# Performance work log

Hardware: AMD Instinct MI355X
Metric: run time of the kernel (lower is better)

## Reference

```python
import jax, jax.numpy as jnp
import numpy as np

PACK = 8  # 32-bit words / 4-bit weights
GROUP = 128


def _unpack4(q):
    # q: [E, K//8, N] int32 packed nibbles -> [E, K, N] ints in [0, 15]
    nib = jnp.stack([(q >> (4 * j)) & 0xF for j in range(PACK)], axis=2)
    E, Kp, _, N = nib.shape
    return nib.reshape(E, Kp * PACK, N)


def _dequant(qweight, scales, g_idx):
    # GPTQ symmetric 4-bit: w = (nibble - 8) * scale[group(k), n]
    # g_idx (desc_act) maps each input row k to its quantization group,
    # equivalent math to Marlin's sorted-g_idx activation reordering.
    w = _unpack4(qweight).astype(jnp.float32) - 8.0          # [E, K, N]
    s = jnp.take_along_axis(scales, g_idx[:, :, None].astype(jnp.int32), axis=1)
    return w * s


def reference(x, router_logits, w13_qweight, w2_qweight,
              w13_scales, w2_scales, w13_g_idx, w2_g_idx, top_k):
    T = x.shape[0]
    E = w13_qweight.shape[0]
    W13 = _dequant(w13_qweight, w13_scales, w13_g_idx)   # [E, H, 2I]
    W2 = _dequant(w2_qweight, w2_scales, w2_g_idx)       # [E, I, H]
    I = W2.shape[1]

    # routing: softmax -> top-k -> renormalize
    probs = jax.nn.softmax(router_logits, axis=-1)       # [T, E]
    tw, tid = jax.lax.top_k(probs, top_k)                # [T, k]
    tw = tw / jnp.sum(tw, axis=-1, keepdims=True)
    cw = jnp.zeros((T, E), x.dtype).at[jnp.arange(T)[:, None], tid].add(tw)

    # grouped GEMM over all experts, weighted combine
    h = jnp.einsum('th,ehn->etn', x, W13)                # [E, T, 2I]
    gate, up = h[..., :I], h[..., I:]
    act = jax.nn.silu(gate) * up                         # [E, T, I]
    out_e = jnp.einsum('eti,eih->eth', act, W2)          # [E, T, H]
    return jnp.einsum('eth,te->th', out_e, cw)           # [T, H]


def setup_inputs() -> dict:
    key = jax.random.key(0)
    ks = jax.random.split(key, 8)
    T, E, H, I = 2048, 8, 1024, 4096
    x = jax.random.normal(ks[0], (T, H), dtype=jnp.float32)
    router_logits = jax.random.normal(ks[1], (T, E), dtype=jnp.float32)
    w13_qweight = jax.random.randint(ks[2], (E, H // PACK, 2 * I), 0, 2147483647, dtype=jnp.int32)
    w2_qweight = jax.random.randint(ks[3], (E, I // PACK, H), 0, 2147483647, dtype=jnp.int32)
    w13_scales = jax.random.uniform(ks[4], (E, H // GROUP, 2 * I), dtype=jnp.float32) * 0.02
    w2_scales = jax.random.uniform(ks[5], (E, I // GROUP, H), dtype=jnp.float32) * 0.02
    w13_g_idx = jax.random.randint(ks[6], (E, H), 0, H // GROUP, dtype=jnp.int32)
    w2_g_idx = jax.random.randint(ks[7], (E, I), 0, I // GROUP, dtype=jnp.int32)
    return {
        'x': x, 'router_logits': router_logits,
        'w13_qweight': w13_qweight, 'w2_qweight': w2_qweight,
        'w13_scales': w13_scales, 'w2_scales': w2_scales,
        'w13_g_idx': w13_g_idx, 'w2_g_idx': w2_g_idx,
        'top_k': 2,
    }
```

## Files before the change

### kernel.cpp

```cpp
#include <hip/hip_runtime.h>

#define T_TOK 2048
#define NEXP  8
#define H_DIM 1024
#define I_DIM 4096

#define N13  (2*I_DIM)
#define N2   (H_DIM)
#define NG13 8
#define NG2  32

#define KSPLIT2 4
#define KLEN2 (I_DIM/KSPLIT2)
#define BK   64

#define MAXT1 24
#define MAXT2 40

typedef __bf16 bf16x8 __attribute__((ext_vector_type(8)));
typedef float  f32x4  __attribute__((ext_vector_type(4)));

#define GLD_LDS(g, l) \
  __builtin_amdgcn_global_load_lds((const __attribute__((address_space(1))) void*)(g), \
                                   (__attribute__((address_space(3))) void*)(l), 16, 0, 0)

#define WS_COUNTS 0
#define WS_OFFS   64
#define WS_CURS   128
#define WS_TOKE   256
#define WS_TOKW   (WS_TOKE  + 2*T_TOK*4)
#define WS_PLIST  (WS_TOKW  + 2*T_TOK*4)
#define WS_PW     (WS_PLIST + 2*T_TOK*4)
#define WS_WL1    65792
#define WS_WL2    65920
#define WS_NTS    66176
#define PAIR_PAD  (2*T_TOK + 128)
#define WS_XG     131072
#define WS_ACT    (WS_XG  + PAIR_PAD*H_DIM*2)
#define WS_B1T    (WS_ACT + (size_t)PAIR_PAD*I_DIM*2)
#define WS_W2T    (WS_B1T + (size_t)NEXP*N13*H_DIM*2)

__global__ void k_route(const float* __restrict__ logits,
                        int* __restrict__ counts,
                        int* __restrict__ tok_e, float* __restrict__ tok_w) {
    int t = blockIdx.x * blockDim.x + threadIdx.x;
    if (t >= T_TOK) return;
    float l[NEXP];
    #pragma unroll
    for (int e = 0; e < NEXP; e++) l[e] = logits[t * NEXP + e];
    int i0 = 0; float b0 = l[0];
    #pragma unroll
    for (int e = 1; e < NEXP; e++) if (l[e] > b0) { b0 = l[e]; i0 = e; }
    int i1 = -1; float b1 = -1e30f;
    #pragma unroll
    for (int e = 0; e < NEXP; e++) if (e != i0 && l[e] > b1) { b1 = l[e]; i1 = e; }
    float w1 = 1.f / (1.f + __expf(b0 - b1));
    float w0 = 1.f - w1;
    tok_e[2*t] = i0; tok_e[2*t+1] = i1;
    tok_w[2*t] = w0; tok_w[2*t+1] = w1;
    atomicAdd(&counts[i0], 1);
    atomicAdd(&counts[i1], 1);
}

__global__ void k_scan(const int* __restrict__ counts,
                       int* __restrict__ offs, int* __restrict__ curs,
                       int* __restrict__ wl1, int* __restrict__ wl2,
                       int* __restrict__ nts) {
    if (threadIdx.x == 0) {
        int s = 0;
        for (int e = 0; e < NEXP; e++) { offs[e] = s; curs[e] = s; s += counts[e]; }
        offs[NEXP] = s;
        int n1 = 0, n2 = 0;
        for (int e = 0; e < NEXP; e++) {
            int c = counts[e];
            for (int mt = 0; mt * 256 < c; mt++) wl1[n1++] = (e << 8) | mt;
            for (int mt = 0; mt * 128 < c; mt++) wl2[n2++] = (e << 8) | mt;
        }
        nts[0] = n1; nts[1] = n2;
    }
}

__global__ void k_scatter(const int* __restrict__ tok_e, const float* __restrict__ tok_w,
                          int* __restrict__ curs,
                          int* __restrict__ plist, float* __restrict__ pw) {
    int t = blockIdx.x * blockDim.x + threadIdx.x;
    if (t >= T_TOK) return;
    #pragma unroll
    for (int s = 0; s < 2; s++) {
        int e = tok_e[2*t+s];
        int pos = atomicAdd(&curs[e], 1);
        plist[pos] = t;
        pw[pos] = tok_w[2*t+s];
    }
}

__global__ void k_gather(const float* __restrict__ x, const int* __restrict__ plist,
                         __bf16* __restrict__ xg) {
    int p = blockIdx.x;
    int t = plist[p];
    int i = threadIdx.x;
    const f32x4* src = reinterpret_cast<const f32x4*>(x + (size_t)t * H_DIM);
    f32x4 v0 = src[i*2], v1 = src[i*2+1];
    __align__(16) __bf16 tb[8];
    #pragma unroll
    for (int j = 0; j < 4; j++) { tb[j] = (__bf16)v0[j]; tb[4+j] = (__bf16)v1[j]; }
    *reinterpret_cast<f32x4*>(xg + (size_t)p * H_DIM + i*8) = *reinterpret_cast<f32x4*>(tb);
}

template<bool INTERLEAVE>
__global__ __launch_bounds__(256) void k_dequant(
    const int* __restrict__ q, const float* __restrict__ s, const int* __restrict__ g,
    __bf16* __restrict__ outw, int R, int K, int N, int NG) {

    const int e  = blockIdx.z;
    const int r0 = blockIdx.x * 64;
    const int k0 = blockIdx.y * 128;
    const int*   qe = q + (size_t)e * (K/8) * N;
    const float* se = s + (size_t)e * NG * N;
    const int*   ge = g + (size_t)e * K + k0;
    __bf16*      oe = outw + (size_t)e * R * K;

    __shared__ __align__(16) __bf16 tile[64][128];

    const int t  = threadIdx.x;
    const int rl = t & 63, kq = t >> 6;
    const int r  = r0 + rl;
    const int S  = INTERLEAVE ? (((r >> 4) << 3) + (r & 7) + (((r >> 3) & 1) ? (N >> 1) : 0))
                              : r;
    #pragma unroll
    for (int jj = 0; jj < 4; jj++) {
        int kp = kq + jj*4;
        int qv = qe[(size_t)(k0/8 + kp) * N + S];
        __align__(16) __bf16 tmp[8];
        #pragma unroll
        for (int j2 = 0; j2 < 8; j2++) {
            float sc = se[(size_t)ge[kp*8 + j2] * N + S];
            tmp[j2] = (__bf16)((float)(((qv >> (4*j2)) & 15) - 8) * sc);
        }
        int c = kp ^ (rl & 15);
        *reinterpret_cast<f32x4*>(&tile[rl][c*8]) = *reinterpret_cast<f32x4*>(tmp);
    }
    __syncthreads();
    #pragma unroll
    for (int i = 0; i < 4; i++) {
        int sidx = t + i*256;
        int row = sidx >> 4, ch = sidx & 15;
        int cs = ch ^ (row & 15);
        *reinterpret_cast<f32x4*>(oe + (size_t)(r0+row)*K + k0 + ch*8)
            = *reinterpret_cast<const f32x4*>(&tile[row][cs*8]);
    }
}

#define VM4 asm volatile("s_waitcnt vmcnt(4)" ::: "memory")
#define VM3 asm volatile("s_waitcnt vmcnt(3)" ::: "memory")
#define VM0 asm volatile("s_waitcnt vmcnt(0)" ::: "memory")
#define LGK0 { asm volatile("s_waitcnt lgkmcnt(0)" ::: "memory"); __builtin_amdgcn_sched_barrier(0); }
#define BARRIER  { __builtin_amdgcn_s_barrier(); __builtin_amdgcn_sched_barrier(0); }
#define SCHEDFENCE __builtin_amdgcn_sched_barrier(0)

__global__ __launch_bounds__(512) void k_gemm1(
    const __bf16* __restrict__ xg,
    const __bf16* __restrict__ B1t,
    const int*    __restrict__ offs,
    const float*  __restrict__ pw,
    const int*    __restrict__ wl1,
    const int*    __restrict__ nts,
    __bf16*       __restrict__ act) {

    const int ti = blockIdx.x >> 5;
    const int nb = blockIdx.x & 31;
    if (ti >= nts[0]) return;
    const int w  = wl1[ti];
    const int e  = w >> 8, mt = w & 255;
    const int m0 = offs[e] + mt * 256;
    const int mcount = min(offs[e+1] - m0, 256);
    const int n0r = nb * 256;

    __shared__ __align__(16) __bf16 AsF[2*2*8192];
    __shared__ __align__(16) __bf16 BsF[2*2*8192];
    __shared__ float wts[256];

    const int tid = threadIdx.x;
    const int wv = tid >> 6, lane = tid & 63;
    const int lrow = lane & 15, quad = lane >> 4;
    const int wr = (wv >> 2) * 128;
    const int wc = (wv & 3) * 64;
    const int cq = quad ^ ((lrow >> 1) & 3);

    for (int m = tid; m < 256; m += 512)
        wts[m] = (m < mcount) ? pw[m0 + m] : 0.f;

    const __bf16* Abase = xg  + (size_t)m0 * H_DIM;
    const __bf16* Bbase = B1t + ((size_t)e * N13 + n0r) * H_DIM;

    f32x4 acc[8][4];
    #pragma unroll
    for (int i = 0; i < 8; i++)
        #pragma unroll
        for (int j = 0; j < 4; j++) acc[i][j] = (f32x4)(0.f);

    auto stageA = [&](int prt, int h2, int kt) {
        const __bf16* g = Abase + kt * BK + h2 * 32;
        __bf16* d = AsF + prt * 16384 + h2 * 8192;
        #pragma unroll
        for (int q2 = 0; q2 < 2; q2++) {
            int row = (tid >> 2) + q2 * 128;
            int gch = (tid & 3) ^ ((row >> 1) & 3);
            int rowc = min(row, mcount - 1);
            GLD_LDS(g + (size_t)rowc * H_DIM + gch * 8, d + tid * 8 + q2 * 4096);
        }
    };
    auto stageB = [&](int prt, int h2, int kt) {
        const __bf16* g = Bbase + kt * BK + h2 * 32;
        __bf16* d = BsF + prt * 16384 + h2 * 8192;
        #pragma unroll
        for (int q2 = 0; q2 < 2; q2++) {
            int row = (tid >> 2) + q2 * 128;
            int gch = (tid & 3) ^ ((row >> 1) & 3);
            GLD_LDS(g + (size_t)row * H_DIM + gch * 8, d + tid * 8 + q2 * 4096);
        }
    };

    stageA(0, 0, 0); stageB(0, 0, 0); stageA(0, 1, 0); stageB(0, 1, 0);

    const int NT = H_DIM / BK;
    for (int kt = 0; kt < NT; kt++) {
        const int prt = kt & 1, nxt = prt ^ 1;
        const bool st = (kt + 1 < NT);
        const __bf16* Ab = AsF + prt * 16384;
        const __bf16* Bb = BsF + prt * 16384;
        #pragma unroll
        for (int h2 = 0; h2 < 2; h2++) {
            bf16x8 bb[4];
            if (h2 == 0) { VM4; } else if (st) { VM4; } else { VM0; }
            BARRIER;
            {
                #pragma unroll
                for (int j = 0; j < 4; j++)
                    bb[j] = *reinterpret_cast<const bf16x8*>(
                        &Bb[h2*8192 + (wc + 16*j + lrow)*32 + cq*8]);
                bf16x8 a[4];
                #pragma unroll
                for (int i = 0; i < 4; i++)
                    a[i] = *reinterpret_cast<const bf16x8*>(
                        &Ab[h2*8192 + (wr + 16*i + lrow)*32 + cq*8]);
                if (st) stageA(nxt, h2, kt + 1);
                LGK0;
                __builtin_amdgcn_s_setprio(1);
                #pragma unroll
                for (int j = 0; j < 4; j++)
                    #pragma unroll
                    for (int i = 0; i < 4; i++)
                        acc[i][j] = __builtin_amdgcn_mfma_f32_16x16x32_bf16(a[i], bb[j], acc[i][j], 0, 0, 0);
                __builtin_amdgcn_s_setprio(0);
            }
            SCHEDFENCE;
            BARRIER;
            {
                bf16x8 a[4];
                #pragma unroll
                for (int i = 0; i < 4; i++)
                    a[i] = *reinterpret_cast<const bf16x8*>(
                        &Ab[h2*8192 + (wr + 64 + 16*i + lrow)*32 + cq*8]);
                if (st) stageB(nxt, h2, kt + 1);
                LGK0;
                __builtin_amdgcn_s_setprio(1);
                #pragma unroll
                for (int j = 0; j < 4; j++)
                    #pragma unroll
                    for (int i = 0; i < 4; i++)
                        acc[4+i][j] = __builtin_amdgcn_mfma_f32_16x16x32_bf16(a[i], bb[j], acc[4+i][j], 0, 0, 0);
                __builtin_amdgcn_s_setprio(0);
            }
            SCHEDFENCE;
        }
    }

    #pragma unroll
    for (int j = 0; j < 4; j++) {
        const int c0 = ((n0r + wc + 16*j) >> 1);
        #pragma unroll
        for (int i = 0; i < 8; i++)
            #pragma unroll
            for (int rr = 0; rr < 4; rr++) {
                float v = acc[i][j][rr];
                float partner = __shfl_xor(v, 8, 64);
                int m = wr + 16*i + quad*4 + rr;
                if (lrow < 8 && m < mcount) {
                    float gg = v, uu = partner;
                    float a = (gg / (1.f + __expf(-gg))) * uu * wts[m];
                    act[(size_t)(m0 + m) * I_DIM + c0 + lrow] = (__bf16)a;
                }
            }
    }
}

__global__ __launch_bounds__(512) void k_gemm2(
    const __bf16* __restrict__ act,
    const __bf16* __restrict__ W2t,
    const int*    __restrict__ offs,
    const int*    __restrict__ plist,
    const int*    __restrict__ wl2,
    const int*    __restrict__ nts,
    float*        __restrict__ out) {

    const int ti = blockIdx.x >> 4;
    if (ti >= nts[1]) return;
    const int nb = (blockIdx.x >> 2) & 3;
    const int ks = blockIdx.x & 3;
    const int w  = wl2[ti];
    const int e  = w >> 8, mt = w & 255;
    const int m0 = offs[e] + mt * 128;
    const int mcount = min(offs[e+1] - m0, 128);
    const int n0 = nb * 256;
    const int kz = ks * KLEN2;

    __shared__ __align__(16) __bf16 AsF[2*2*4096];
    __shared__ __align__(16) __bf16 BsF[2*2*8192];
    __shared__ int toks[128];

    const int tid = threadIdx.x;
    const int wv = tid >> 6, lane = tid & 63;
    const int lrow = lane & 15, quad = lane >> 4;
    const int wr = (wv >> 2) * 64;
    const int wc = (wv & 3) * 64;
    const int cq = quad ^ ((lrow >> 1) & 3);

    for (int m = tid; m < 128; m += 512)
        toks[m] = (m < mcount) ? plist[m0 + m] : 0;

    const __bf16* Abase = act + (size_t)m0 * I_DIM + kz;
    const __bf16* Bbase = W2t + ((size_t)e * N2 + n0) * I_DIM + kz;

    f32x4 acc[4][4];
    #pragma unroll
    for (int i = 0; i < 4; i++)
        #pragma unroll
        for (int j = 0; j < 4; j++) acc[i][j] = (f32x4)(0.f);

    auto stageA = [&](int prt, int h2, int kt) {
        const __bf16* g = Abase + kt * BK + h2 * 32;
        __bf16* d = AsF + prt * 8192 + h2 * 4096;
        int row = tid >> 2;
        int gch = (tid & 3) ^ ((row >> 1) & 3);
        int rowc = min(row, mcount - 1);
        GLD_LDS(g + (size_t)rowc * I_DIM + gch * 8, d + tid * 8);
    };
    auto stageB = [&](int prt, int h2, int kt) {
        const __bf16* g = Bbase + kt * BK + h2 * 32;
        __bf16* d = BsF + prt * 16384 + h2 * 8192;
        #pragma unroll
        for (int q2 = 0; q2 < 2; q2++) {
            int row = (tid >> 2) + q2 * 128;
            int gch = (tid & 3) ^ ((row >> 1) & 3);
            GLD_LDS(g + (size_t)row * I_DIM + gch * 8, d + tid * 8 + q2 * 4096);
        }
    };

    stageA(0, 0, 0); stageB(0, 0, 0); stageA(0, 1, 0); stageB(0, 1, 0);

    const int NT = KLEN2 / BK;
    for (int kt = 0; kt < NT; kt++) {
        const int prt = kt & 1, nxt = prt ^ 1;
        const bool st = (kt + 1 < NT);
        const __bf16* Ab = AsF + prt * 8192;
        const __bf16* Bb = BsF + prt * 16384;
        #pragma unroll
        for (int h2 = 0; h2 < 2; h2++) {
            if (h2 == 0) { VM3; } else if (st) { VM3; } else { VM0; }
            BARRIER;
            {
                bf16x8 bb[4], a[4];
                #pragma unroll
                for (int j = 0; j < 4; j++)
                    bb[j] = *reinterpret_cast<const bf16x8*>(
                        &Bb[h2*8192 + (wc + 16*j + lrow)*32 + cq*8]);
                #pragma unroll
                for (int i = 0; i < 4; i++)
                    a[i] = *reinterpret_cast<const bf16x8*>(
                        &Ab[h2*4096 + (wr + 16*i + lrow)*32 + cq*8]);
                if (st) { stageA(nxt, h2, kt + 1); stageB(nxt, h2, kt + 1); }
                LGK0;
                __builtin_amdgcn_s_setprio(1);
                #pragma unroll
                for (int j = 0; j < 4; j++)
                    #pragma unroll
                    for (int i = 0; i < 4; i++)
                        acc[i][j] = __builtin_amdgcn_mfma_f32_16x16x32_bf16(a[i], bb[j], acc[i][j], 0, 0, 0);
                __builtin_amdgcn_s_setprio(0);
            }
            SCHEDFENCE;
        }
    }

    #pragma unroll
    for (int j = 0; j < 4; j++) {
        int h = n0 + wc + 16*j + lrow;
        #pragma unroll
        for (int i = 0; i < 4; i++)
            #pragma unroll
            for (int rr = 0; rr < 4; rr++) {
                int m = wr + 16*i + quad*4 + rr;
                if (m < mcount)
                    atomicAdd(&out[(size_t)toks[m] * H_DIM + h], acc[i][j][rr]);
            }
    }
}

extern "C" void kernel_launch(void* const* d_in, const int* in_sizes, int n_in,
                              void* d_out, int out_size, void* d_ws, size_t ws_size,
                              hipStream_t stream) {
    const float* x      = (const float*)d_in[0];
    const float* logits = (const float*)d_in[1];
    const int*   w13q   = (const int*)  d_in[2];
    const int*   w2q    = (const int*)  d_in[3];
    const float* w13s   = (const float*)d_in[4];
    const float* w2s    = (const float*)d_in[5];
    const int*   g13    = (const int*)  d_in[6];
    const int*   g2     = (const int*)  d_in[7];

    char* ws = (char*)d_ws;
    int*    counts = (int*)   (ws + WS_COUNTS);
    int*    offs   = (int*)   (ws + WS_OFFS);
    int*    curs   = (int*)   (ws + WS_CURS);
    int*    tok_e  = (int*)   (ws + WS_TOKE);
    float*  tok_w  = (float*) (ws + WS_TOKW);
    int*    plist  = (int*)   (ws + WS_PLIST);
    float*  pw     = (float*) (ws + WS_PW);
    int*    wl1    = (int*)   (ws + WS_WL1);
    int*    wl2    = (int*)   (ws + WS_WL2);
    int*    nts    = (int*)   (ws + WS_NTS);
    __bf16* xg     = (__bf16*)(ws + WS_XG);
    __bf16* act    = (__bf16*)(ws + WS_ACT);
    __bf16* B1t    = (__bf16*)(ws + WS_B1T);
    __bf16* W2t    = (__bf16*)(ws + WS_W2T);
    float*  out    = (float*) d_out;

    hipMemsetAsync(d_out, 0, (size_t)out_size * sizeof(float), stream);
    hipMemsetAsync(d_ws, 0, 256, stream);

    k_dequant<true ><<<dim3(N13/64, H_DIM/128, NEXP), 256, 0, stream>>>(
        w13q, w13s, g13, B1t, N13, H_DIM, N13, NG13);
    k_dequant<false><<<dim3(N2/64,  I_DIM/128, NEXP), 256, 0, stream>>>(
        w2q,  w2s,  g2,  W2t, N2,  I_DIM, N2,  NG2);

    k_route  <<<T_TOK/256, 256, 0, stream>>>(logits, counts, tok_e, tok_w);
    k_scan   <<<1, 64, 0, stream>>>(counts, offs, curs, wl1, wl2, nts);
    k_scatter<<<T_TOK/256, 256, 0, stream>>>(tok_e, tok_w, curs, plist, pw);
    k_gather <<<2*T_TOK, 128, 0, stream>>>(x, plist, xg);

    k_gemm1<<<MAXT1 * 32, 512, 0, stream>>>(xg, B1t, offs, pw, wl1, nts, act);
    k_gemm2<<<MAXT2 * 16, 512, 0, stream>>>(act, W2t, offs, plist, wl2, nts, out);
}
```

Before: 432.4 us.

## Shrink gemm1 M-tile to 128 and double gemm2 K-split

The gemm1 token tile drops from 256 to 128 rows, so each K step has one MFMA phase instead of two, and the A buffer and accumulator sets are halved. The routing worklist is unified to 128-row tiles shared by both GEMMs. gemm2's K split goes from 4 to 8, which doubles its grid. Together these are meant to raise occupancy and the number of workgroups on the GPU. In exchange, B-tile reuse per block falls, gemm1 rereads more weight traffic, and gemm2 adds more atomic partial-sum writes.

```diff
diff --git a/kernel.cpp b/kernel.cpp
--- a/kernel.cpp
+++ b/kernel.cpp
@@ -10,11 +10,10 @@
 #define NG13 8
 #define NG2  32
 
-#define KSPLIT2 4
+#define KSPLIT2 8
 #define KLEN2 (I_DIM/KSPLIT2)
 #define BK   64
 
-#define MAXT1 24
 #define MAXT2 40
 
 typedef __bf16 bf16x8 __attribute__((ext_vector_type(8)));
@@ -31,8 +30,7 @@
 #define WS_TOKW   (WS_TOKE  + 2*T_TOK*4)
 #define WS_PLIST  (WS_TOKW  + 2*T_TOK*4)
 #define WS_PW     (WS_PLIST + 2*T_TOK*4)
-#define WS_WL1    65792
-#define WS_WL2    65920
+#define WS_WL     65792
 #define WS_NTS    66176
 #define PAIR_PAD  (2*T_TOK + 128)
 #define WS_XG     131072
@@ -64,19 +62,17 @@
 
 __global__ void k_scan(const int* __restrict__ counts,
                        int* __restrict__ offs, int* __restrict__ curs,
-                       int* __restrict__ wl1, int* __restrict__ wl2,
-                       int* __restrict__ nts) {
+                       int* __restrict__ wl, int* __restrict__ nts) {
     if (threadIdx.x == 0) {
         int s = 0;
         for (int e = 0; e < NEXP; e++) { offs[e] = s; curs[e] = s; s += counts[e]; }
         offs[NEXP] = s;
-        int n1 = 0, n2 = 0;
+        int n = 0;
         for (int e = 0; e < NEXP; e++) {
             int c = counts[e];
-            for (int mt = 0; mt * 256 < c; mt++) wl1[n1++] = (e << 8) | mt;
-            for (int mt = 0; mt * 128 < c; mt++) wl2[n2++] = (e << 8) | mt;
-        }
-        nts[0] = n1; nts[1] = n2;
+            for (int mt = 0; mt * 128 < c; mt++) wl[n++] = (e << 8) | mt;
+        }
+        nts[0] = n;
     }
 }
 
@@ -151,7 +147,6 @@
     }
 }
 
-#define VM4 asm volatile("s_waitcnt vmcnt(4)" ::: "memory")
 #define VM3 asm volatile("s_waitcnt vmcnt(3)" ::: "memory")
 #define VM0 asm volatile("s_waitcnt vmcnt(0)" ::: "memory")
 #define LGK0 { asm volatile("s_waitcnt lgkmcnt(0)" ::: "memory"); __builtin_amdgcn_sched_barrier(0); }
@@ -163,52 +158,49 @@
     const __bf16* __restrict__ B1t,
     const int*    __restrict__ offs,
     const float*  __restrict__ pw,
-    const int*    __restrict__ wl1,
+    const int*    __restrict__ wl,
     const int*    __restrict__ nts,
     __bf16*       __restrict__ act) {
 
     const int ti = blockIdx.x >> 5;
+    if (ti >= nts[0]) return;
     const int nb = blockIdx.x & 31;
-    if (ti >= nts[0]) return;
-    const int w  = wl1[ti];
+    const int w  = wl[ti];
     const int e  = w >> 8, mt = w & 255;
-    const int m0 = offs[e] + mt * 256;
-    const int mcount = min(offs[e+1] - m0, 256);
+    const int m0 = offs[e] + mt * 128;
+    const int mcount = min(offs[e+1] - m0, 128);
     const int n0r = nb * 256;
 
-    __shared__ __align__(16) __bf16 AsF[2*2*8192];
+    __shared__ __align__(16) __bf16 AsF[2*2*4096];
     __shared__ __align__(16) __bf16 BsF[2*2*8192];
-    __shared__ float wts[256];
+    __shared__ float wts[128];
 
     const int tid = threadIdx.x;
     const int wv = tid >> 6, lane = tid & 63;
     const int lrow = lane & 15, quad = lane >> 4;
-    const int wr = (wv >> 2) * 128;
+    const int wr = (wv >> 2) * 64;
     const int wc = (wv & 3) * 64;
     const int cq = quad ^ ((lrow >> 1) & 3);
 
-    for (int m = tid; m < 256; m += 512)
+    for (int m = tid; m < 128; m += 512)
         wts[m] = (m < mcount) ? pw[m0 + m] : 0.f;
 
     const __bf16* Abase = xg  + (size_t)m0 * H_DIM;
     const __bf16* Bbase = B1t + ((size_t)e * N13 + n0r) * H_DIM;
 
-    f32x4 acc[8][4];
-    #pragma unroll
-    for (int i = 0; i < 8; i++)
+    f32x4 acc[4][4];
+    #pragma unroll
+    for (int i = 0; i < 4; i++)
         #pragma unroll
         for (int j = 0; j < 4; j++) acc[i][j] = (f32x4)(0.f);
 
     auto stageA = [&](int prt, int h2, int kt) {
         const __bf16* g = Abase + kt * BK + h2 * 32;
-        __bf16* d = AsF + prt * 16384 + h2 * 8192;
-        #pragma unroll
-        for (int q2 = 0; q2 < 2; q2++) {
-            int row = (tid >> 2) + q2 * 128;
-            int gch = (tid & 3) ^ ((row >> 1) & 3);
-            int rowc = min(row, mcount - 1);
-            GLD_LDS(g + (size_t)rowc * H_DIM + gch * 8, d + tid * 8 + q2 * 4096);
-        }
+        __bf16* d = AsF + prt * 8192 + h2 * 4096;
+        int row = tid >> 2;
+        int gch = (tid & 3) ^ ((row >> 1) & 3);
+        int rowc = min(row, mcount - 1);
+        GLD_LDS(g + (size_t)rowc * H_DIM + gch * 8, d + tid * 8);
     };
     auto stageB = [&](int prt, int h2, int kt) {
         const __bf16* g = Bbase + kt * BK + h2 * 32;
@@ -227,24 +219,23 @@
     for (int kt = 0; kt < NT; kt++) {
         const int prt = kt & 1, nxt = prt ^ 1;
         const bool st = (kt + 1 < NT);
-        const __bf16* Ab = AsF + prt * 16384;
+        const __bf16* Ab = AsF + prt * 8192;
         const __bf16* Bb = BsF + prt * 16384;
         #pragma unroll
         for (int h2 = 0; h2 < 2; h2++) {
-            bf16x8 bb[4];
-            if (h2 == 0) { VM4; } else if (st) { VM4; } else { VM0; }
+            if (h2 == 0) { VM3; } else if (st) { VM3; } else { VM0; }
             BARRIER;
             {
+                bf16x8 bb[4], a[4];
                 #pragma unroll
                 for (int j = 0; j < 4; j++)
                     bb[j] = *reinterpret_cast<const bf16x8*>(
                         &Bb[h2*8192 + (wc + 16*j + lrow)*32 + cq*8]);
-                bf16x8 a[4];
                 #pragma unroll
                 for (int i = 0; i < 4; i++)
                     a[i] = *reinterpret_cast<const bf16x8*>(
-                        &Ab[h2*8192 + (wr + 16*i + lrow)*32 + cq*8]);
-                if (st) stageA(nxt, h2, kt + 1);
+                        &Ab[h2*4096 + (wr + 16*i + lrow)*32 + cq*8]);
+                if (st) { stageA(nxt, h2, kt + 1); stageB(nxt, h2, kt + 1); }
                 LGK0;
                 __builtin_amdgcn_s_setprio(1);
                 #pragma unroll
@@ -255,24 +246,6 @@
                 __builtin_amdgcn_s_setprio(0);
             }
             SCHEDFENCE;
-            BARRIER;
-            {
-                bf16x8 a[4];
-                #pragma unroll
-                for (int i = 0; i < 4; i++)
-                    a[i] = *reinterpret_cast<const bf16x8*>(
-                        &Ab[h2*8192 + (wr + 64 + 16*i + lrow)*32 + cq*8]);
-                if (st) stageB(nxt, h2, kt + 1);
-                LGK0;
-                __builtin_amdgcn_s_setprio(1);
-                #pragma unroll
-                for (int j = 0; j < 4; j++)
-                    #pragma unroll
-                    for (int i = 0; i < 4; i++)
-                        acc[4+i][j] = __builtin_amdgcn_mfma_f32_16x16x32_bf16(a[i], bb[j], acc[4+i][j], 0, 0, 0);
-                __builtin_amdgcn_s_setprio(0);
-            }
-            SCHEDFENCE;
         }
     }
 
@@ -280,7 +253,7 @@
     for (int j = 0; j < 4; j++) {
         const int c0 = ((n0r + wc + 16*j) >> 1);
         #pragma unroll
-        for (int i = 0; i < 8; i++)
+        for (int i = 0; i < 4; i++)
             #pragma unroll
             for (int rr = 0; rr < 4; rr++) {
                 float v = acc[i][j][rr];
@@ -300,15 +273,15 @@
     const __bf16* __restrict__ W2t,
     const int*    __restrict__ offs,
     const int*    __restrict__ plist,
-    const int*    __restrict__ wl2,
+    const int*    __restrict__ wl,
     const int*    __restrict__ nts,
     float*        __restrict__ out) {
 
-    const int ti = blockIdx.x >> 4;
-    if (ti >= nts[1]) return;
-    const int nb = (blockIdx.x >> 2) & 3;
-    const int ks = blockIdx.x & 3;
-    const int w  = wl2[ti];
+    const int ti = blockIdx.x >> 5;
+    if (ti >= nts[0]) return;
+    const int nb = (blockIdx.x >> 3) & 3;
+    const int ks = blockIdx.x & 7;
+    const int w  = wl[ti];
     const int e  = w >> 8, mt = w & 255;
     const int m0 = offs[e] + mt * 128;
     const int mcount = min(offs[e+1] - m0, 128);
@@ -427,8 +400,7 @@
     float*  tok_w  = (float*) (ws + WS_TOKW);
     int*    plist  = (int*)   (ws + WS_PLIST);
     float*  pw     = (float*) (ws + WS_PW);
-    int*    wl1    = (int*)   (ws + WS_WL1);
-    int*    wl2    = (int*)   (ws + WS_WL2);
+    int*    wl     = (int*)   (ws + WS_WL);
     int*    nts    = (int*)   (ws + WS_NTS);
     __bf16* xg     = (__bf16*)(ws + WS_XG);
     __bf16* act    = (__bf16*)(ws + WS_ACT);
@@ -445,10 +417,10 @@
         w2q,  w2s,  g2,  W2t, N2,  I_DIM, N2,  NG2);
 
     k_route  <<<T_TOK/256, 256, 0, stream>>>(logits, counts, tok_e, tok_w);
-    k_scan   <<<1, 64, 0, stream>>>(counts, offs, curs, wl1, wl2, nts);
+    k_scan   <<<1, 64, 0, stream>>>(counts, offs, curs, wl, nts);
     k_scatter<<<T_TOK/256, 256, 0, stream>>>(tok_e, tok_w, curs, plist, pw);
     k_gather <<<2*T_TOK, 128, 0, stream>>>(x, plist, xg);
 
-    k_gemm1<<<MAXT1 * 32, 512, 0, stream>>>(xg, B1t, offs, pw, wl1, nts, act);
-    k_gemm2<<<MAXT2 * 16, 512, 0, stream>>>(act, W2t, offs, plist, wl2, nts, out);
-}
+    k_gemm1<<<MAXT2 * 32, 512, 0, stream>>>(xg, B1t, offs, pw, wl, nts, act);
+    k_gemm2<<<MAXT2 * 32, 512, 0, stream>>>(act, W2t, offs, plist, wl, nts, out);
+}
```

Measured after the change: 464.0 us. 7.3% more time.
